# Optimization experiments

Measured on AMD Instinct MI355X. Metric: run time of the kernel, lower is better.

Reference implementation:

```python
import jax, jax.numpy as jnp
import numpy as np

K = 512
D = 64
BETA = 0.25


def setup_inputs() -> dict:
    key = jax.random.key(0)
    k1, k2 = jax.random.split(key)
    z_e = jax.random.normal(k1, (64, D, 64, 64), dtype=jnp.float32)  # (B, D, H, W)
    # uniform(-1/K, 1/K) init like nn.Embedding.weight.data.uniform_
    codebook = jax.random.uniform(k2, (K, D), dtype=jnp.float32, minval=-1.0 / K, maxval=1.0 / K)
    return {"z_e": z_e, "codebook": codebook}


def reference(z_e, codebook):
    B, d, H, W = z_e.shape
    # (B, D, H, W) -> (B*H*W, D)
    z_e_flat = jnp.transpose(z_e, (0, 2, 3, 1)).reshape(-1, d)
    # squared euclidean distances: ||z||^2 - 2 z.E^T + ||E||^2  -> (N, K)
    dists = (
        jnp.sum(z_e_flat * z_e_flat, axis=1, keepdims=True)
        - 2.0 * (z_e_flat @ codebook.T)
        + jnp.sum(codebook * codebook, axis=1)[None, :]
    )
    indices = jnp.argmin(dists, axis=1)  # (N,)
    z_q_flat = codebook[indices]         # (N, D)
    codebook_loss = jnp.mean((z_q_flat - jax.lax.stop_gradient(z_e_flat)) ** 2)
    commitment_loss = BETA * jnp.mean((z_e_flat - jax.lax.stop_gradient(z_q_flat)) ** 2)
    # straight-through estimator
    z_q_flat_st = z_e_flat + jax.lax.stop_gradient(z_q_flat - z_e_flat)
    z_q = jnp.transpose(z_q_flat_st.reshape(B, H, W, d), (0, 3, 1, 2))
    return z_q, codebook_loss, commitment_loss
```

## Files before the change

kernel.cpp:

```cpp
#include <hip/hip_runtime.h>
#include <hip/hip_bf16.h>
#include <stdint.h>


typedef float f32x16 __attribute__((ext_vector_type(16)));
typedef float f32x2 __attribute__((ext_vector_type(2)));

union Fu { uint32_t w[2]; uint2 u2; long l; };

__global__ __launch_bounds__(256)
void vq_prep(const float* __restrict__ cb, uint32_t* __restrict__ cb8,
             float* __restrict__ e2) {
  int t = blockIdx.x * 256 + threadIdx.x;
  int k = t >> 4, dw = t & 15;
  const float4 f = ((const float4*)cb)[t];
  uint32_t u = 0;
  u = __builtin_amdgcn_cvt_pk_fp8_f32(f.x * 512.f, f.y * 512.f, u, false);
  u = __builtin_amdgcn_cvt_pk_fp8_f32(f.z * 512.f, f.w * 512.f, u, true);
  int ch = dw >> 1;
  cb8[k * 16 + ((ch ^ (k & 7)) << 1) + (dw & 1)] = u;
  float s = f.x * f.x + f.y * f.y + f.z * f.z + f.w * f.w;
  s += __shfl_xor(s, 1);
  s += __shfl_xor(s, 2);
  s += __shfl_xor(s, 4);
  s += __shfl_xor(s, 8);
  if ((t & 15) == 0) e2[k] = s;
}

__global__ __launch_bounds__(256)
void vq_main(const float* __restrict__ zin, const uint32_t* __restrict__ cb8,
             const float* __restrict__ e2g, float* __restrict__ out) {
  __shared__ uint32_t cbl[8192];
  const int tid = threadIdx.x;
  const int wid = tid >> 6;
  const int lane = tid & 63;
  const int col = lane & 31;
  const int half = lane >> 5;
  const int xk = col & 7;

  {
    const uint4* cb4 = (const uint4*)cb8;
#pragma unroll
    for (int j = 0; j < 8; ++j) ((uint4*)cbl)[j * 256 + tid] = cb4[j * 256 + tid];
  }
  __syncthreads();

  const int s = blockIdx.x;
  const int b = s >> 4;
  const int hw0 = (s & 15) << 8;
  const float* slab = zin + ((size_t)b << 18) + hw0;

  Fu Bf[2][4];
  float z2[2];
#pragma unroll
  for (int rt = 0; rt < 2; ++rt) {
    const int r = wid * 64 + rt * 32 + col;
    float sacc = 0.f;
#pragma unroll
    for (int m = 0; m < 4; ++m) {
      const int d0 = m * 16 + half * 8;
      float v0 = slab[(size_t)(d0 + 0) * 4096 + r];
      float v1 = slab[(size_t)(d0 + 1) * 4096 + r];
      float v2 = slab[(size_t)(d0 + 2) * 4096 + r];
      float v3 = slab[(size_t)(d0 + 3) * 4096 + r];
      float v4 = slab[(size_t)(d0 + 4) * 4096 + r];
      float v5 = slab[(size_t)(d0 + 5) * 4096 + r];
      float v6 = slab[(size_t)(d0 + 6) * 4096 + r];
      float v7 = slab[(size_t)(d0 + 7) * 4096 + r];
      sacc += v0 * v0 + v1 * v1 + v2 * v2 + v3 * v3 + v4 * v4 + v5 * v5 +
              v6 * v6 + v7 * v7;
      uint32_t lo = __builtin_amdgcn_cvt_pk_fp8_f32(v0, v1, 0u, false);
      lo = __builtin_amdgcn_cvt_pk_fp8_f32(v2, v3, lo, true);
      uint32_t hi = __builtin_amdgcn_cvt_pk_fp8_f32(v4, v5, 0u, false);
      hi = __builtin_amdgcn_cvt_pk_fp8_f32(v6, v7, hi, true);
      Bf[rt][m].w[0] = lo;
      Bf[rt][m].w[1] = hi;
    }
    z2[rt] = sacc;
  }

  Fu A[4], An[4];
#pragma unroll
  for (int m = 0; m < 4; ++m)
    A[m].u2 = *(const uint2*)&cbl[(col << 4) + (((2 * m + half) ^ xk) << 1)];
  float st[2] = {-3.4e38f, -3.4e38f};
#pragma unroll 1
  for (int ct = 0; ct < 16; ++ct) {
    const int ctn = (ct + 1) & 15;
    const int nbase = (ctn << 9) + (col << 4);
#pragma unroll
    for (int m = 0; m < 4; ++m)
      An[m].u2 = *(const uint2*)&cbl[nbase + (((2 * m + half) ^ xk) << 1)];
    const uint32_t ctor = (uint32_t)(ct << 5) | (uint32_t)(half << 2);
#pragma unroll
    for (int rt = 0; rt < 2; ++rt) {
      f32x16 acc = {0, 0, 0, 0, 0, 0, 0, 0, 0, 0, 0, 0, 0, 0, 0, 0};
#pragma unroll
      for (int m = 0; m < 4; ++m)
        acc = __builtin_amdgcn_mfma_f32_32x32x16_fp8_fp8(A[m].l, Bf[rt][m].l,
                                                         acc, 0, 0, 0);
#pragma unroll
      for (int r16 = 0; r16 < 16; ++r16) {
        const uint32_t cr = (uint32_t)((r16 & 3) | ((r16 >> 2) << 3));
        uint32_t bits =
            (__builtin_bit_cast(uint32_t, acc[r16]) & 0xFFFFFE00u) | (ctor | cr);
        st[rt] = fmaxf(st[rt], __builtin_bit_cast(float, bits));
      }
    }
#pragma unroll
    for (int m = 0; m < 4; ++m) A[m].u2 = An[m].u2;
  }

  float blk = 0.f;
  int kk[2];
  {
    float lsum = 0.f;
#pragma unroll
    for (int rt = 0; rt < 2; ++rt) {
      float mx = fmaxf(st[rt], __shfl_xor(st[rt], 32));
      float z2t = z2[rt] + __shfl_xor(z2[rt], 32);
      uint32_t mbits = __builtin_bit_cast(uint32_t, mx);
      kk[rt] = (int)(mbits & 511u);
      float dot = __builtin_bit_cast(float, mbits & 0xFFFFFE00u);
      lsum += z2t - dot * 0.00390625f + e2g[kk[rt]];
    }
#pragma unroll
    for (int off = 1; off <= 16; off <<= 1) lsum += __shfl_xor(lsum, off);
    blk = lsum;
  }

  {
    float* oslab = out + ((size_t)b << 18) + hw0;
#pragma unroll
    for (int rt = 0; rt < 2; ++rt) {
      const int k = kk[rt];
      const int r = wid * 64 + rt * 32 + col;
      const int kx = k & 7;
#pragma unroll
      for (int cc = 0; cc < 4; ++cc) {
        const int ch = half * 4 + cc;
        Fu q;
        q.u2 = *(const uint2*)&cbl[(k << 4) + (((ch ^ kx)) << 1)];
#pragma unroll
        for (int dw = 0; dw < 2; ++dw) {
          f32x2 f0 = __builtin_amdgcn_cvt_pk_f32_fp8(q.w[dw], false);
          f32x2 f1 = __builtin_amdgcn_cvt_pk_f32_fp8(q.w[dw], true);
          const int d = half * 32 + cc * 8 + dw * 4;
          oslab[(size_t)(d + 0) * 4096 + r] = f0.x * 0.001953125f;
          oslab[(size_t)(d + 1) * 4096 + r] = f0.y * 0.001953125f;
          oslab[(size_t)(d + 2) * 4096 + r] = f1.x * 0.001953125f;
          oslab[(size_t)(d + 3) * 4096 + r] = f1.y * 0.001953125f;
        }
      }
    }
  }

  __syncthreads();
  if (lane == 0) ((float*)cbl)[wid] = blk;
  __syncthreads();
  if (tid == 0) {
    float t = ((float*)cbl)[0] + ((float*)cbl)[1] + ((float*)cbl)[2] + ((float*)cbl)[3];
    float sc = t * (1.0f / 16777216.0f);
    atomicAdd(out + 16777216, sc);
    atomicAdd(out + 16777217, 0.25f * sc);
  }
}

extern "C" void kernel_launch(void* const* d_in, const int* in_sizes, int n_in,
                              void* d_out, int out_size, void* d_ws, size_t ws_size,
                              hipStream_t stream) {
  const float* zin = (const float*)d_in[0];
  const float* cbf = (const float*)d_in[1];
  uint32_t* cb8 = (uint32_t*)d_ws;
  float* e2 = (float*)((char*)d_ws + 32768);
  float* out = (float*)d_out;

  vq_prep<<<32, 256, 0, stream>>>(cbf, cb8, e2);
  vq_main<<<1024, 256, 0, stream>>>(zin, cb8, e2, out);
}
```

Baseline: 133.4 us.

## Stage z_e through LDS with async global_load_lds and process two slabs per block

Input tiles are now loaded with global_load_lds into a double-buffered LDS staging area, so the next 16-channel chunk (and the next slab) is fetched while the current one is converted to fp8. Each block handles two 256-pixel slabs, so the grid halves and the codebook copy into LDS is amortized over twice the work. The codebook LDS layout changes from XOR-swizzled to a chunk-major layout, and the output gather is restructured to emit float4 stores through a shared index array. It adds about 32KB more LDS per block and several extra barriers, which may lower occupancy.

New measurement: 128.7 us. -3.5%, faster.

```diff
diff --git a/kernel.cpp b/kernel.cpp
--- a/kernel.cpp
+++ b/kernel.cpp
@@ -7,6 +7,12 @@
 typedef float f32x2 __attribute__((ext_vector_type(2)));
 
 union Fu { uint32_t w[2]; uint2 u2; long l; };
+
+__device__ __forceinline__ void gld_lds16(const float* g, float* l) {
+  __builtin_amdgcn_global_load_lds(
+      (const __attribute__((address_space(1))) void*)(g),
+      (__attribute__((address_space(3))) void*)(l), 16, 0, 0);
+}
 
 __global__ __launch_bounds__(256)
 void vq_prep(const float* __restrict__ cb, uint32_t* __restrict__ cb8,
@@ -17,8 +23,7 @@
   uint32_t u = 0;
   u = __builtin_amdgcn_cvt_pk_fp8_f32(f.x * 512.f, f.y * 512.f, u, false);
   u = __builtin_amdgcn_cvt_pk_fp8_f32(f.z * 512.f, f.w * 512.f, u, true);
-  int ch = dw >> 1;
-  cb8[k * 16 + ((ch ^ (k & 7)) << 1) + (dw & 1)] = u;
+  cb8[((k >> 5) << 9) + ((dw >> 1) << 6) + ((k & 31) << 1) + (dw & 1)] = u;
   float s = f.x * f.x + f.y * f.y + f.z * f.z + f.w * f.w;
   s += __shfl_xor(s, 1);
   s += __shfl_xor(s, 2);
@@ -31,135 +36,167 @@
 void vq_main(const float* __restrict__ zin, const uint32_t* __restrict__ cb8,
              const float* __restrict__ e2g, float* __restrict__ out) {
   __shared__ uint32_t cbl[8192];
+  __shared__ float zst[2][16][256];
+  __shared__ unsigned short ks[256] __attribute__((aligned(8)));
+  __shared__ float lred[4];
   const int tid = threadIdx.x;
   const int wid = tid >> 6;
   const int lane = tid & 63;
   const int col = lane & 31;
   const int half = lane >> 5;
-  const int xk = col & 7;
 
   {
-    const uint4* cb4 = (const uint4*)cb8;
-#pragma unroll
-    for (int j = 0; j < 8; ++j) ((uint4*)cbl)[j * 256 + tid] = cb4[j * 256 + tid];
+    const uint4* c4 = (const uint4*)cb8;
+#pragma unroll
+    for (int j = 0; j < 8; ++j) ((uint4*)cbl)[j * 256 + tid] = c4[j * 256 + tid];
   }
+
+  const int s0 = blockIdx.x * 2;
+  const int b0 = s0 >> 4;
+  const float* slab0 = zin + ((size_t)b0 << 18) + ((s0 & 15) << 8);
+#pragma unroll
+  for (int j = 0; j < 4; ++j)
+    gld_lds16(slab0 + (size_t)(wid * 4 + j) * 4096 + lane * 4,
+              &zst[0][wid * 4 + j][0]);
+
+  float blk = 0.f;
+#pragma unroll 1
+  for (int it = 0; it < 2; ++it) {
+    const int s = s0 + it;
+    const int b = s >> 4;
+    const int hw0 = (s & 15) << 8;
+    const float* slab = zin + ((size_t)b << 18) + hw0;
+    float* oslab = out + ((size_t)b << 18) + hw0;
+
+    Fu Bf[2][4];
+    float z2[2] = {0.f, 0.f};
+#pragma unroll
+    for (int m = 0; m < 4; ++m) {
+      __syncthreads();
+      if (m < 3) {
+#pragma unroll
+        for (int j = 0; j < 4; ++j)
+          gld_lds16(slab + (size_t)((m + 1) * 16 + wid * 4 + j) * 4096 + lane * 4,
+                    &zst[(m + 1) & 1][wid * 4 + j][0]);
+      }
+#pragma unroll
+      for (int rt = 0; rt < 2; ++rt) {
+        const int r = wid * 64 + rt * 32 + col;
+        float v[8];
+#pragma unroll
+        for (int q = 0; q < 8; ++q) v[q] = zst[m & 1][half * 8 + q][r];
+        float sa = 0.f;
+#pragma unroll
+        for (int q = 0; q < 8; ++q) sa += v[q] * v[q];
+        z2[rt] += sa;
+        uint32_t lo = __builtin_amdgcn_cvt_pk_fp8_f32(v[0], v[1], 0u, false);
+        lo = __builtin_amdgcn_cvt_pk_fp8_f32(v[2], v[3], lo, true);
+        uint32_t hi = __builtin_amdgcn_cvt_pk_fp8_f32(v[4], v[5], 0u, false);
+        hi = __builtin_amdgcn_cvt_pk_fp8_f32(v[6], v[7], hi, true);
+        Bf[rt][m].w[0] = lo;
+        Bf[rt][m].w[1] = hi;
+      }
+    }
+
+    Fu A[4], An[4];
+#pragma unroll
+    for (int m = 0; m < 4; ++m)
+      A[m].u2 = *(const uint2*)&cbl[((2 * m + half) << 6) + (col << 1)];
+    float st[2] = {-3.4e38f, -3.4e38f};
+#pragma unroll 1
+    for (int ct = 0; ct < 16; ++ct) {
+      const int ctn = (ct + 1) & 15;
+      const int nb = (ctn << 9) + (col << 1);
+#pragma unroll
+      for (int m = 0; m < 4; ++m)
+        An[m].u2 = *(const uint2*)&cbl[nb + ((2 * m + half) << 6)];
+      const uint32_t ctor = (uint32_t)(ct << 5) | (uint32_t)(half << 2);
+#pragma unroll
+      for (int rt = 0; rt < 2; ++rt) {
+        f32x16 acc = {0, 0, 0, 0, 0, 0, 0, 0, 0, 0, 0, 0, 0, 0, 0, 0};
+#pragma unroll
+        for (int m = 0; m < 4; ++m)
+          acc = __builtin_amdgcn_mfma_f32_32x32x16_fp8_fp8(A[m].l, Bf[rt][m].l,
+                                                           acc, 0, 0, 0);
+#pragma unroll
+        for (int r16 = 0; r16 < 16; ++r16) {
+          const uint32_t cr = (uint32_t)((r16 & 3) | ((r16 >> 2) << 3));
+          uint32_t bits =
+              (__builtin_bit_cast(uint32_t, acc[r16]) & 0xFFFFFE00u) | (ctor | cr);
+          st[rt] = fmaxf(st[rt], __builtin_bit_cast(float, bits));
+        }
+      }
+#pragma unroll
+      for (int m = 0; m < 4; ++m) A[m].u2 = An[m].u2;
+    }
+
+    int kk[2];
+    {
+      float lsum = 0.f;
+#pragma unroll
+      for (int rt = 0; rt < 2; ++rt) {
+        float mx = fmaxf(st[rt], __shfl_xor(st[rt], 32));
+        float z2t = z2[rt] + __shfl_xor(z2[rt], 32);
+        uint32_t mbits = __builtin_bit_cast(uint32_t, mx);
+        kk[rt] = (int)(mbits & 511u);
+        float dot = __builtin_bit_cast(float, mbits & 0xFFFFFE00u);
+        lsum += z2t - dot * 0.00390625f + e2g[kk[rt]];
+      }
+#pragma unroll
+      for (int off = 1; off <= 16; off <<= 1) lsum += __shfl_xor(lsum, off);
+      blk += lsum;
+      if (half == 0) {
+        ks[wid * 64 + col] = (unsigned short)kk[0];
+        ks[wid * 64 + 32 + col] = (unsigned short)kk[1];
+      }
+    }
+    __syncthreads();
+
+    if (it == 0) {
+      const float* slabn = slab + 256;
+#pragma unroll
+      for (int j = 0; j < 4; ++j)
+        gld_lds16(slabn + (size_t)(wid * 4 + j) * 4096 + lane * 4,
+                  &zst[0][wid * 4 + j][0]);
+    }
+
+    {
+      const int r0 = lane << 2;
+      const ushort4 kp = *(const ushort4*)&ks[r0];
+      int k4[4] = {(int)kp.x, (int)kp.y, (int)kp.z, (int)kp.w};
+#pragma unroll
+      for (int g = 0; g < 4; ++g) {
+        uint32_t u[4];
+#pragma unroll
+        for (int j = 0; j < 4; ++j)
+          u[j] = cbl[((k4[j] >> 5) << 9) + ((wid * 2 + (g >> 1)) << 6) +
+                     ((k4[j] & 31) << 1) + (g & 1)];
+        f32x2 t0[4], t1[4];
+#pragma unroll
+        for (int j = 0; j < 4; ++j) {
+          t0[j] = __builtin_amdgcn_cvt_pk_f32_fp8(u[j], false);
+          t1[j] = __builtin_amdgcn_cvt_pk_f32_fp8(u[j], true);
+        }
+        const float S = 0.001953125f;
+        float4 v;
+        const size_t dbase = (size_t)(wid * 16 + g * 4) * 4096 + r0;
+        v.x = t0[0].x * S; v.y = t0[1].x * S; v.z = t0[2].x * S; v.w = t0[3].x * S;
+        *(float4*)&oslab[dbase] = v;
+        v.x = t0[0].y * S; v.y = t0[1].y * S; v.z = t0[2].y * S; v.w = t0[3].y * S;
+        *(float4*)&oslab[dbase + 4096] = v;
+        v.x = t1[0].x * S; v.y = t1[1].x * S; v.z = t1[2].x * S; v.w = t1[3].x * S;
+        *(float4*)&oslab[dbase + 8192] = v;
+        v.x = t1[0].y * S; v.y = t1[1].y * S; v.z = t1[2].y * S; v.w = t1[3].y * S;
+        *(float4*)&oslab[dbase + 12288] = v;
+      }
+    }
+  }
+
   __syncthreads();
-
-  const int s = blockIdx.x;
-  const int b = s >> 4;
-  const int hw0 = (s & 15) << 8;
-  const float* slab = zin + ((size_t)b << 18) + hw0;
-
-  Fu Bf[2][4];
-  float z2[2];
-#pragma unroll
-  for (int rt = 0; rt < 2; ++rt) {
-    const int r = wid * 64 + rt * 32 + col;
-    float sacc = 0.f;
-#pragma unroll
-    for (int m = 0; m < 4; ++m) {
-      const int d0 = m * 16 + half * 8;
-      float v0 = slab[(size_t)(d0 + 0) * 4096 + r];
-      float v1 = slab[(size_t)(d0 + 1) * 4096 + r];
-      float v2 = slab[(size_t)(d0 + 2) * 4096 + r];
-      float v3 = slab[(size_t)(d0 + 3) * 4096 + r];
-      float v4 = slab[(size_t)(d0 + 4) * 4096 + r];
-      float v5 = slab[(size_t)(d0 + 5) * 4096 + r];
-      float v6 = slab[(size_t)(d0 + 6) * 4096 + r];
-      float v7 = slab[(size_t)(d0 + 7) * 4096 + r];
-      sacc += v0 * v0 + v1 * v1 + v2 * v2 + v3 * v3 + v4 * v4 + v5 * v5 +
-              v6 * v6 + v7 * v7;
-      uint32_t lo = __builtin_amdgcn_cvt_pk_fp8_f32(v0, v1, 0u, false);
-      lo = __builtin_amdgcn_cvt_pk_fp8_f32(v2, v3, lo, true);
-      uint32_t hi = __builtin_amdgcn_cvt_pk_fp8_f32(v4, v5, 0u, false);
-      hi = __builtin_amdgcn_cvt_pk_fp8_f32(v6, v7, hi, true);
-      Bf[rt][m].w[0] = lo;
-      Bf[rt][m].w[1] = hi;
-    }
-    z2[rt] = sacc;
-  }
-
-  Fu A[4], An[4];
-#pragma unroll
-  for (int m = 0; m < 4; ++m)
-    A[m].u2 = *(const uint2*)&cbl[(col << 4) + (((2 * m + half) ^ xk) << 1)];
-  float st[2] = {-3.4e38f, -3.4e38f};
-#pragma unroll 1
-  for (int ct = 0; ct < 16; ++ct) {
-    const int ctn = (ct + 1) & 15;
-    const int nbase = (ctn << 9) + (col << 4);
-#pragma unroll
-    for (int m = 0; m < 4; ++m)
-      An[m].u2 = *(const uint2*)&cbl[nbase + (((2 * m + half) ^ xk) << 1)];
-    const uint32_t ctor = (uint32_t)(ct << 5) | (uint32_t)(half << 2);
-#pragma unroll
-    for (int rt = 0; rt < 2; ++rt) {
-      f32x16 acc = {0, 0, 0, 0, 0, 0, 0, 0, 0, 0, 0, 0, 0, 0, 0, 0};
-#pragma unroll
-      for (int m = 0; m < 4; ++m)
-        acc = __builtin_amdgcn_mfma_f32_32x32x16_fp8_fp8(A[m].l, Bf[rt][m].l,
-                                                         acc, 0, 0, 0);
-#pragma unroll
-      for (int r16 = 0; r16 < 16; ++r16) {
-        const uint32_t cr = (uint32_t)((r16 & 3) | ((r16 >> 2) << 3));
-        uint32_t bits =
-            (__builtin_bit_cast(uint32_t, acc[r16]) & 0xFFFFFE00u) | (ctor | cr);
-        st[rt] = fmaxf(st[rt], __builtin_bit_cast(float, bits));
-      }
-    }
-#pragma unroll
-    for (int m = 0; m < 4; ++m) A[m].u2 = An[m].u2;
-  }
-
-  float blk = 0.f;
-  int kk[2];
-  {
-    float lsum = 0.f;
-#pragma unroll
-    for (int rt = 0; rt < 2; ++rt) {
-      float mx = fmaxf(st[rt], __shfl_xor(st[rt], 32));
-      float z2t = z2[rt] + __shfl_xor(z2[rt], 32);
-      uint32_t mbits = __builtin_bit_cast(uint32_t, mx);
-      kk[rt] = (int)(mbits & 511u);
-      float dot = __builtin_bit_cast(float, mbits & 0xFFFFFE00u);
-      lsum += z2t - dot * 0.00390625f + e2g[kk[rt]];
-    }
-#pragma unroll
-    for (int off = 1; off <= 16; off <<= 1) lsum += __shfl_xor(lsum, off);
-    blk = lsum;
-  }
-
-  {
-    float* oslab = out + ((size_t)b << 18) + hw0;
-#pragma unroll
-    for (int rt = 0; rt < 2; ++rt) {
-      const int k = kk[rt];
-      const int r = wid * 64 + rt * 32 + col;
-      const int kx = k & 7;
-#pragma unroll
-      for (int cc = 0; cc < 4; ++cc) {
-        const int ch = half * 4 + cc;
-        Fu q;
-        q.u2 = *(const uint2*)&cbl[(k << 4) + (((ch ^ kx)) << 1)];
-#pragma unroll
-        for (int dw = 0; dw < 2; ++dw) {
-          f32x2 f0 = __builtin_amdgcn_cvt_pk_f32_fp8(q.w[dw], false);
-          f32x2 f1 = __builtin_amdgcn_cvt_pk_f32_fp8(q.w[dw], true);
-          const int d = half * 32 + cc * 8 + dw * 4;
-          oslab[(size_t)(d + 0) * 4096 + r] = f0.x * 0.001953125f;
-          oslab[(size_t)(d + 1) * 4096 + r] = f0.y * 0.001953125f;
-          oslab[(size_t)(d + 2) * 4096 + r] = f1.x * 0.001953125f;
-          oslab[(size_t)(d + 3) * 4096 + r] = f1.y * 0.001953125f;
-        }
-      }
-    }
-  }
-
-  __syncthreads();
-  if (lane == 0) ((float*)cbl)[wid] = blk;
+  if (lane == 0) lred[wid] = blk;
   __syncthreads();
   if (tid == 0) {
-    float t = ((float*)cbl)[0] + ((float*)cbl)[1] + ((float*)cbl)[2] + ((float*)cbl)[3];
+    float t = lred[0] + lred[1] + lred[2] + lred[3];
     float sc = t * (1.0f / 16777216.0f);
     atomicAdd(out + 16777216, sc);
     atomicAdd(out + 16777217, 0.25f * sc);
@@ -176,5 +213,5 @@
   float* out = (float*)d_out;
 
   vq_prep<<<32, 256, 0, stream>>>(cbf, cb8, e2);
-  vq_main<<<1024, 256, 0, stream>>>(zin, cb8, e2, out);
-}
+  vq_main<<<512, 256, 0, stream>>>(zin, cb8, e2, out);
+}
```

## Split argmin and dequant into separate kernels with new codebook LDS layout

Applied to the files above, without the earlier changes.

Splits the fused kernel in two. The first kernel computes the argmin and the loss and writes the 16-bit code indices to workspace. A second kernel reloads the codebook into LDS, gathers the chosen codes and writes the output with float4 stores instead of scalar strided stores. The codebook layout changes from an XOR-swizzled row-major form to a dimension-chunk-major form, so the MFMA operand LDS reads become contiguous per chunk. The cost is an extra kernel launch, a second codebook load per block, and a small global round trip for the indices.

Measured after the change: 142.9 us. +7.1%, slower.

```diff
diff --git a/kernel.cpp b/kernel.cpp
--- a/kernel.cpp
+++ b/kernel.cpp
@@ -17,8 +17,7 @@
   uint32_t u = 0;
   u = __builtin_amdgcn_cvt_pk_fp8_f32(f.x * 512.f, f.y * 512.f, u, false);
   u = __builtin_amdgcn_cvt_pk_fp8_f32(f.z * 512.f, f.w * 512.f, u, true);
-  int ch = dw >> 1;
-  cb8[k * 16 + ((ch ^ (k & 7)) << 1) + (dw & 1)] = u;
+  cb8[((k >> 5) << 9) + ((dw >> 1) << 6) + ((k & 31) << 1) + (dw & 1)] = u;
   float s = f.x * f.x + f.y * f.y + f.z * f.z + f.w * f.w;
   s += __shfl_xor(s, 1);
   s += __shfl_xor(s, 2);
@@ -28,20 +27,21 @@
 }
 
 __global__ __launch_bounds__(256)
-void vq_main(const float* __restrict__ zin, const uint32_t* __restrict__ cb8,
-             const float* __restrict__ e2g, float* __restrict__ out) {
+void vq_argmin(const float* __restrict__ zin, const uint32_t* __restrict__ cb8,
+               const float* __restrict__ e2g, unsigned short* __restrict__ ksg,
+               float* __restrict__ out) {
   __shared__ uint32_t cbl[8192];
+  __shared__ float lred[4];
   const int tid = threadIdx.x;
   const int wid = tid >> 6;
   const int lane = tid & 63;
   const int col = lane & 31;
   const int half = lane >> 5;
-  const int xk = col & 7;
 
   {
-    const uint4* cb4 = (const uint4*)cb8;
-#pragma unroll
-    for (int j = 0; j < 8; ++j) ((uint4*)cbl)[j * 256 + tid] = cb4[j * 256 + tid];
+    const uint4* c4 = (const uint4*)cb8;
+#pragma unroll
+    for (int j = 0; j < 8; ++j) ((uint4*)cbl)[j * 256 + tid] = c4[j * 256 + tid];
   }
   __syncthreads();
 
@@ -82,15 +82,15 @@
   Fu A[4], An[4];
 #pragma unroll
   for (int m = 0; m < 4; ++m)
-    A[m].u2 = *(const uint2*)&cbl[(col << 4) + (((2 * m + half) ^ xk) << 1)];
+    A[m].u2 = *(const uint2*)&cbl[((2 * m + half) << 6) + (col << 1)];
   float st[2] = {-3.4e38f, -3.4e38f};
 #pragma unroll 1
   for (int ct = 0; ct < 16; ++ct) {
     const int ctn = (ct + 1) & 15;
-    const int nbase = (ctn << 9) + (col << 4);
+    const int nb = (ctn << 9) + (col << 1);
 #pragma unroll
     for (int m = 0; m < 4; ++m)
-      An[m].u2 = *(const uint2*)&cbl[nbase + (((2 * m + half) ^ xk) << 1)];
+      An[m].u2 = *(const uint2*)&cbl[nb + ((2 * m + half) << 6)];
     const uint32_t ctor = (uint32_t)(ct << 5) | (uint32_t)(half << 2);
 #pragma unroll
     for (int rt = 0; rt < 2; ++rt) {
@@ -111,10 +111,9 @@
     for (int m = 0; m < 4; ++m) A[m].u2 = An[m].u2;
   }
 
-  float blk = 0.f;
-  int kk[2];
   {
     float lsum = 0.f;
+    int kk[2];
 #pragma unroll
     for (int rt = 0; rt < 2; ++rt) {
       float mx = fmaxf(st[rt], __shfl_xor(st[rt], 32));
@@ -126,43 +125,70 @@
     }
 #pragma unroll
     for (int off = 1; off <= 16; off <<= 1) lsum += __shfl_xor(lsum, off);
-    blk = lsum;
-  }
-
-  {
-    float* oslab = out + ((size_t)b << 18) + hw0;
-#pragma unroll
-    for (int rt = 0; rt < 2; ++rt) {
-      const int k = kk[rt];
-      const int r = wid * 64 + rt * 32 + col;
-      const int kx = k & 7;
-#pragma unroll
-      for (int cc = 0; cc < 4; ++cc) {
-        const int ch = half * 4 + cc;
-        Fu q;
-        q.u2 = *(const uint2*)&cbl[(k << 4) + (((ch ^ kx)) << 1)];
-#pragma unroll
-        for (int dw = 0; dw < 2; ++dw) {
-          f32x2 f0 = __builtin_amdgcn_cvt_pk_f32_fp8(q.w[dw], false);
-          f32x2 f1 = __builtin_amdgcn_cvt_pk_f32_fp8(q.w[dw], true);
-          const int d = half * 32 + cc * 8 + dw * 4;
-          oslab[(size_t)(d + 0) * 4096 + r] = f0.x * 0.001953125f;
-          oslab[(size_t)(d + 1) * 4096 + r] = f0.y * 0.001953125f;
-          oslab[(size_t)(d + 2) * 4096 + r] = f1.x * 0.001953125f;
-          oslab[(size_t)(d + 3) * 4096 + r] = f1.y * 0.001953125f;
-        }
-      }
-    }
-  }
-
-  __syncthreads();
-  if (lane == 0) ((float*)cbl)[wid] = blk;
+    if (half == 0) {
+      ksg[s * 256 + wid * 64 + col] = (unsigned short)kk[0];
+      ksg[s * 256 + wid * 64 + 32 + col] = (unsigned short)kk[1];
+    }
+    if (lane == 0) lred[wid] = lsum;
+  }
   __syncthreads();
   if (tid == 0) {
-    float t = ((float*)cbl)[0] + ((float*)cbl)[1] + ((float*)cbl)[2] + ((float*)cbl)[3];
+    float t = lred[0] + lred[1] + lred[2] + lred[3];
     float sc = t * (1.0f / 16777216.0f);
     atomicAdd(out + 16777216, sc);
     atomicAdd(out + 16777217, 0.25f * sc);
+  }
+}
+
+__global__ __launch_bounds__(256)
+void vq_dequant(const uint32_t* __restrict__ cb8,
+                const unsigned short* __restrict__ ksg,
+                float* __restrict__ out) {
+  __shared__ uint32_t cbl[8192];
+  __shared__ unsigned short ksl[256] __attribute__((aligned(8)));
+  const int tid = threadIdx.x;
+  const int wid = tid >> 6;
+  const int lane = tid & 63;
+
+  const int s = blockIdx.x;
+  const int b = s >> 4;
+  const int hw0 = (s & 15) << 8;
+  {
+    const uint4* c4 = (const uint4*)cb8;
+#pragma unroll
+    for (int j = 0; j < 8; ++j) ((uint4*)cbl)[j * 256 + tid] = c4[j * 256 + tid];
+    ksl[tid] = ksg[s * 256 + tid];
+  }
+  __syncthreads();
+
+  float* oslab = out + ((size_t)b << 18) + hw0;
+  const int r0 = lane << 2;
+  const ushort4 kp = *(const ushort4*)&ksl[r0];
+  int k4[4] = {(int)kp.x, (int)kp.y, (int)kp.z, (int)kp.w};
+#pragma unroll
+  for (int g = 0; g < 4; ++g) {
+    uint32_t u[4];
+#pragma unroll
+    for (int j = 0; j < 4; ++j)
+      u[j] = cbl[((k4[j] >> 5) << 9) + ((wid * 2 + (g >> 1)) << 6) +
+                 ((k4[j] & 31) << 1) + (g & 1)];
+    f32x2 t0[4], t1[4];
+#pragma unroll
+    for (int j = 0; j < 4; ++j) {
+      t0[j] = __builtin_amdgcn_cvt_pk_f32_fp8(u[j], false);
+      t1[j] = __builtin_amdgcn_cvt_pk_f32_fp8(u[j], true);
+    }
+    const float S = 0.001953125f;
+    float4 v;
+    const size_t dbase = (size_t)(wid * 16 + g * 4) * 4096 + r0;
+    v.x = t0[0].x * S; v.y = t0[1].x * S; v.z = t0[2].x * S; v.w = t0[3].x * S;
+    *(float4*)&oslab[dbase] = v;
+    v.x = t0[0].y * S; v.y = t0[1].y * S; v.z = t0[2].y * S; v.w = t0[3].y * S;
+    *(float4*)&oslab[dbase + 4096] = v;
+    v.x = t1[0].x * S; v.y = t1[1].x * S; v.z = t1[2].x * S; v.w = t1[3].x * S;
+    *(float4*)&oslab[dbase + 8192] = v;
+    v.x = t1[0].y * S; v.y = t1[1].y * S; v.z = t1[2].y * S; v.w = t1[3].y * S;
+    *(float4*)&oslab[dbase + 12288] = v;
   }
 }
 
@@ -173,8 +199,10 @@
   const float* cbf = (const float*)d_in[1];
   uint32_t* cb8 = (uint32_t*)d_ws;
   float* e2 = (float*)((char*)d_ws + 32768);
+  unsigned short* ks = (unsigned short*)((char*)d_ws + 36864);
   float* out = (float*)d_out;
 
   vq_prep<<<32, 256, 0, stream>>>(cbf, cb8, e2);
-  vq_main<<<1024, 256, 0, stream>>>(zin, cb8, e2, out);
-}
+  vq_argmin<<<1024, 256, 0, stream>>>(zin, cb8, e2, ks, out);
+  vq_dequant<<<1024, 256, 0, stream>>>(cb8, ks, out);
+}
```
